# Kernel optimization log

Measured on AMD Instinct MI355X. Metric: run time of the kernel, lower is better.

## Reference

```python
import jax, jax.numpy as jnp
import numpy as np

HIDDEN = 1024
NUM_HEADS = 16
HEAD_SIZE = HIDDEN // NUM_HEADS
B, S = 2, 2048


def setup_inputs() -> dict:
    key = jax.random.key(0)
    k_x, k_wqkv, k_bqkv, k_wo, k_bo = jax.random.split(key, 5)
    x = jax.random.normal(k_x, (B, S, HIDDEN), dtype=jnp.float32)
    # Dense kernels, fan-in scaled like lecun_normal init
    Wqkv = jax.random.normal(k_wqkv, (HIDDEN, 3 * HIDDEN), dtype=jnp.float32) / np.sqrt(HIDDEN)
    bqkv = jnp.zeros((3 * HIDDEN,), dtype=jnp.float32)
    Wo = jax.random.normal(k_wo, (HIDDEN, HIDDEN), dtype=jnp.float32) / np.sqrt(HIDDEN)
    bo = jnp.zeros((HIDDEN,), dtype=jnp.float32)
    return {"x": x, "Wqkv": Wqkv, "bqkv": bqkv, "Wo": Wo, "bo": bo}


def reference(x, Wqkv, bqkv, Wo, bo):
    b, s, h = x.shape
    qkv = jnp.einsum('bsh,hf->bsf', x, Wqkv) + bqkv          # [b, s, 3*h]
    qkv = qkv.reshape(b, s, 3, NUM_HEADS, HEAD_SIZE)
    q, k, v = qkv[:, :, 0], qkv[:, :, 1], qkv[:, :, 2]        # [b, s, nh, hd]
    scale = 1.0 / np.sqrt(HEAD_SIZE)
    scores = jnp.einsum('bqhd,bkhd->bhqk', q, k) * scale      # [b, nh, s, s]
    weights = jax.nn.softmax(scores, axis=-1)
    attn = jnp.einsum('bhqk,bkhd->bqhd', weights, v)          # [b, s, nh, hd]
    attn = attn.reshape(b, s, h)
    return jnp.einsum('bsh,hf->bsf', attn, Wo) + bo
```

## Files before the change

### kernel.cpp

```cpp
#include <hip/hip_runtime.h>
#include <hip/hip_bf16.h>

#define HIDDEN 1024
#define NH 16
#define BATCH 2
#define SEQ 2048

typedef __attribute__((ext_vector_type(8))) short bf16x8;
typedef __attribute__((ext_vector_type(4))) float f32x4;

__device__ __forceinline__ ushort f2bf(float f) {
    __hip_bfloat16 h = __float2bfloat16(f);
    return *reinterpret_cast<ushort*>(&h);
}
__device__ __forceinline__ float bf2f(ushort u) {
    __hip_bfloat16 h;
    *reinterpret_cast<ushort*>(&h) = u;
    return __bfloat162float(h);
}

__device__ __forceinline__ void async_copy16(const ushort* g, ushort* l) {
    __builtin_amdgcn_global_load_lds((const __attribute__((address_space(1))) void*)g,
                                     (__attribute__((address_space(3))) void*)l,
                                     16, 0, 0);
}

__global__ void convert_f32_bf16_kernel(const float* __restrict__ in,
                                        ushort* __restrict__ out)
{
    int i = (blockIdx.x * 256 + threadIdx.x) * 4;
    float4 v = *(const float4*)(in + i);
    ushort4 w;
    w.x = f2bf(v.x); w.y = f2bf(v.y); w.z = f2bf(v.z); w.w = f2bf(v.w);
    *(ushort4*)(out + i) = w;
}

__global__ void transpose_f32_bf16_kernel(const float* __restrict__ W,
                                          ushort* __restrict__ Wt,
                                          int K, int N)
{
    __shared__ float t[32][33];
    int k0 = blockIdx.x * 32;
    int n0 = blockIdx.y * 32;
    int r = threadIdx.x >> 3;
    int c = (threadIdx.x & 7) * 4;
    float4 v = *(const float4*)(W + (size_t)(k0 + r) * N + n0 + c);
    t[r][c] = v.x; t[r][c + 1] = v.y; t[r][c + 2] = v.z; t[r][c + 3] = v.w;
    __syncthreads();
    ushort4 w;
    w.x = f2bf(t[c + 0][r]); w.y = f2bf(t[c + 1][r]);
    w.z = f2bf(t[c + 2][r]); w.w = f2bf(t[c + 3][r]);
    *(ushort4*)(Wt + (size_t)(n0 + r) * K + k0 + c) = w;
}

__global__ void transpose_split_bf16_kernel(const float* __restrict__ W,
                                            ushort* __restrict__ Wt_hi,
                                            ushort* __restrict__ Wt_lo,
                                            int K, int N)
{
    __shared__ float t[32][33];
    int k0 = blockIdx.x * 32;
    int n0 = blockIdx.y * 32;
    int r = threadIdx.x >> 3;
    int c = (threadIdx.x & 7) * 4;
    float4 v = *(const float4*)(W + (size_t)(k0 + r) * N + n0 + c);
    t[r][c] = v.x; t[r][c + 1] = v.y; t[r][c + 2] = v.z; t[r][c + 3] = v.w;
    __syncthreads();
    ushort4 whi, wlo;
    float vv;
    vv = t[c + 0][r]; whi.x = f2bf(vv); wlo.x = f2bf(vv - bf2f(whi.x));
    vv = t[c + 1][r]; whi.y = f2bf(vv); wlo.y = f2bf(vv - bf2f(whi.y));
    vv = t[c + 2][r]; whi.z = f2bf(vv); wlo.z = f2bf(vv - bf2f(whi.z));
    vv = t[c + 3][r]; whi.w = f2bf(vv); wlo.w = f2bf(vv - bf2f(whi.w));
    *(ushort4*)(Wt_hi + (size_t)(n0 + r) * K + k0 + c) = whi;
    *(ushort4*)(Wt_lo + (size_t)(n0 + r) * K + k0 + c) = wlo;
}

__global__ void transpose_v_kernel(const ushort* __restrict__ qkvb,
                                   ushort* __restrict__ vtg)
{
    __shared__ ushort T[64][72];
    int blk = blockIdx.x;
    int st = blk & 31;
    int h  = (blk >> 5) & 15;
    int b  = blk >> 9;
    int s0 = st * 64;

    int s  = threadIdx.x >> 2;
    int c0 = (threadIdx.x & 3) * 2;
    const ushort* src = qkvb + ((size_t)(b * SEQ + s0 + s)) * 3072 + 2048 + h * 64;
    *(uint4*)&T[s][c0 * 8]     = *(const uint4*)(src + c0 * 8);
    *(uint4*)&T[s][c0 * 8 + 8] = *(const uint4*)(src + c0 * 8 + 8);
    __syncthreads();

    int d = threadIdx.x >> 2;
    ushort* dst = vtg + ((size_t)((b * NH + h) * 64 + d)) * SEQ + s0;
    #pragma unroll
    for (int cc = 0; cc < 2; cc++) {
        int c2 = (threadIdx.x & 3) * 2 + cc;
        ushort tmp[8];
        #pragma unroll
        for (int j = 0; j < 8; j++) {
            int sp = c2 * 8 + j;
            int key = (sp & 3) * 16 + (sp >> 2);
            tmp[j] = T[key][d];
        }
        *(uint4*)(dst + c2 * 8) = *(const uint4*)tmp;
    }
}

__global__ __launch_bounds__(256, 3)
void gemm_mfma_bf16_kernel(const ushort* __restrict__ A,
                           const ushort* __restrict__ Bt,
                           const float* __restrict__ bias,
                           ushort* __restrict__ C, int N,
                           int qscale_cols)
{
    constexpr int K = 1024;
    __shared__ ushort As[128 * 64];
    __shared__ ushort Bs[128 * 64];

    const int tid  = threadIdx.x;
    const int wave = tid >> 6;
    const int lane = tid & 63;
    const int l16  = lane & 15;
    const int quad = lane >> 4;
    const int wm = wave & 1, wn = wave >> 1;

    const int bm = blockIdx.y * 128;
    const int bn = blockIdx.x * 128;

    const int srow = lane >> 3;
    const int lblk = (lane & 7) ^ srow;
    const ushort* Ag = A  + (size_t)(bm + wave * 32 + srow) * K + lblk * 8;
    const ushort* Bg = Bt + (size_t)(bn + wave * 32 + srow) * K + lblk * 8;
    ushort* Asl = As + wave * 32 * 64;
    ushort* Bsl = Bs + wave * 32 * 64;

    f32x4 acc[4][4];
    #pragma unroll
    for (int i = 0; i < 4; i++)
        #pragma unroll
        for (int j = 0; j < 4; j++) acc[i][j] = (f32x4){0.f, 0.f, 0.f, 0.f};

    for (int k0 = 0; k0 < K; k0 += 64) {
        __syncthreads();
        #pragma unroll
        for (int t = 0; t < 4; t++) {
            async_copy16(Ag + (size_t)t * 8 * K + k0, Asl + t * 8 * 64);
            async_copy16(Bg + (size_t)t * 8 * K + k0, Bsl + t * 8 * 64);
        }
        __syncthreads();

        #pragma unroll
        for (int s = 0; s < 2; s++) {
            bf16x8 af[4], bfr[4];
            #pragma unroll
            for (int i = 0; i < 4; i++) {
                int m = wm * 64 + i * 16 + l16;
                int n = wn * 64 + i * 16 + l16;
                af[i]  = *(const bf16x8*)&As[m * 64 + (((s * 4 + quad) ^ (m & 7)) << 3)];
                bfr[i] = *(const bf16x8*)&Bs[n * 64 + (((s * 4 + quad) ^ (n & 7)) << 3)];
            }
            #pragma unroll
            for (int i = 0; i < 4; i++)
                #pragma unroll
                for (int j = 0; j < 4; j++)
                    acc[i][j] = __builtin_amdgcn_mfma_f32_16x16x32_bf16(af[i], bfr[j], acc[i][j], 0, 0, 0);
        }
    }

    #pragma unroll
    for (int j = 0; j < 4; j++) {
        int col = bn + wn * 64 + j * 16 + l16;
        float bv = bias[col];
        float s = (col < qscale_cols) ? 0.125f : 1.0f;
        #pragma unroll
        for (int i = 0; i < 4; i++) {
            int row0 = bm + wm * 64 + i * 16 + quad * 4;
            #pragma unroll
            for (int r = 0; r < 4; r++)
                C[(size_t)(row0 + r) * N + col] = f2bf((acc[i][j][r] + bv) * s);
        }
    }
}

__global__ __launch_bounds__(256, 2)
void gemm3_split_kernel(const ushort* __restrict__ Ahi,
                        const ushort* __restrict__ Alo,
                        const ushort* __restrict__ Bthi,
                        const ushort* __restrict__ Btlo,
                        const float* __restrict__ bias,
                        float* __restrict__ C)
{
    constexpr int K = 1024, N = 1024;
    __shared__ ushort AsHi[128 * 64];
    __shared__ ushort AsLo[128 * 64];
    __shared__ ushort BsHi[64 * 64];
    __shared__ ushort BsLo[64 * 64];

    const int tid  = threadIdx.x;
    const int wave = tid >> 6;
    const int lane = tid & 63;
    const int l16  = lane & 15;
    const int quad = lane >> 4;
    const int wm = wave & 1, wn = wave >> 1;

    const int bm = blockIdx.y * 128;
    const int bn = blockIdx.x * 64;

    const int srow = lane >> 3;
    const int lblk = (lane & 7) ^ srow;
    const size_t aoff = (size_t)(bm + wave * 32 + srow) * K + lblk * 8;
    const size_t boff = (size_t)(bn + wave * 16 + srow) * K + lblk * 8;
    const ushort* AgHi = Ahi + aoff;
    const ushort* AgLo = Alo + aoff;
    const ushort* BgHi = Bthi + boff;
    const ushort* BgLo = Btlo + boff;
    ushort* AslHi = AsHi + wave * 32 * 64;
    ushort* AslLo = AsLo + wave * 32 * 64;
    ushort* BslHi = BsHi + wave * 16 * 64;
    ushort* BslLo = BsLo + wave * 16 * 64;

    f32x4 acc[4][2];
    #pragma unroll
    for (int i = 0; i < 4; i++)
        #pragma unroll
        for (int j = 0; j < 2; j++) acc[i][j] = (f32x4){0.f, 0.f, 0.f, 0.f};

    for (int k0 = 0; k0 < K; k0 += 64) {
        __syncthreads();
        #pragma unroll
        for (int t = 0; t < 4; t++) {
            async_copy16(AgHi + (size_t)t * 8 * K + k0, AslHi + t * 8 * 64);
            async_copy16(AgLo + (size_t)t * 8 * K + k0, AslLo + t * 8 * 64);
        }
        #pragma unroll
        for (int t = 0; t < 2; t++) {
            async_copy16(BgHi + (size_t)t * 8 * K + k0, BslHi + t * 8 * 64);
            async_copy16(BgLo + (size_t)t * 8 * K + k0, BslLo + t * 8 * 64);
        }
        __syncthreads();

        #pragma unroll
        for (int s = 0; s < 2; s++) {
            bf16x8 ah[4], al[4], bh[2], bl[2];
            #pragma unroll
            for (int i = 0; i < 4; i++) {
                int m = wm * 64 + i * 16 + l16;
                int idx = m * 64 + (((s * 4 + quad) ^ (m & 7)) << 3);
                ah[i] = *(const bf16x8*)&AsHi[idx];
                al[i] = *(const bf16x8*)&AsLo[idx];
            }
            #pragma unroll
            for (int j = 0; j < 2; j++) {
                int n = wn * 32 + j * 16 + l16;
                int idx = n * 64 + (((s * 4 + quad) ^ (n & 7)) << 3);
                bh[j] = *(const bf16x8*)&BsHi[idx];
                bl[j] = *(const bf16x8*)&BsLo[idx];
            }
            #pragma unroll
            for (int i = 0; i < 4; i++)
                #pragma unroll
                for (int j = 0; j < 2; j++) {
                    acc[i][j] = __builtin_amdgcn_mfma_f32_16x16x32_bf16(ah[i], bh[j], acc[i][j], 0, 0, 0);
                    acc[i][j] = __builtin_amdgcn_mfma_f32_16x16x32_bf16(ah[i], bl[j], acc[i][j], 0, 0, 0);
                    acc[i][j] = __builtin_amdgcn_mfma_f32_16x16x32_bf16(al[i], bh[j], acc[i][j], 0, 0, 0);
                }
        }
    }

    #pragma unroll
    for (int j = 0; j < 2; j++) {
        int col = bn + wn * 32 + j * 16 + l16;
        float bv = bias[col];
        #pragma unroll
        for (int i = 0; i < 4; i++) {
            int row0 = bm + wm * 64 + i * 16 + quad * 4;
            #pragma unroll
            for (int r = 0; r < 4; r++)
                C[(size_t)(row0 + r) * N + col] = acc[i][j][r] + bv;
        }
    }
}

__global__ __launch_bounds__(256, 2)
void attn_mfma_kernel(const ushort* __restrict__ qkvb,
                      const ushort* __restrict__ vtg,
                      int use_vtg,
                      ushort* __restrict__ attn_hi,
                      ushort* __restrict__ attn_lo)
{
    __shared__ ushort Ks[64 * 64];
    __shared__ ushort Vs[64 * 64];
    __shared__ ushort Ps[4][32 * 72];

    const int tid  = threadIdx.x;
    const int wave = tid >> 6;
    const int lane = tid & 63;
    const int l16  = lane & 15;
    const int quad = lane >> 4;

    const int qb = blockIdx.x & 15;
    const int bh = blockIdx.x >> 4;
    const int h  = bh & (NH - 1);
    const int b  = bh >> 4;

    const int qbase = qb * 128;
    const int hoff  = h * 64;

    bf16x8 a_q[2][2];
    #pragma unroll
    for (int mg = 0; mg < 2; mg++) {
        int qrow = b * SEQ + qbase + wave * 32 + mg * 16 + l16;
        const ushort* qp = qkvb + (size_t)qrow * 3072 + hoff + quad * 8;
        a_q[mg][0] = *(const bf16x8*)qp;
        a_q[mg][1] = *(const bf16x8*)(qp + 32);
    }

    f32x4 o[2][4];
    f32x4 lacc[2];
    #pragma unroll
    for (int mg = 0; mg < 2; mg++) {
        lacc[mg] = (f32x4){0.f, 0.f, 0.f, 0.f};
        #pragma unroll
        for (int nt = 0; nt < 4; nt++) o[mg][nt] = (f32x4){0.f, 0.f, 0.f, 0.f};
    }

    bf16x8 b_ones;
    #pragma unroll
    for (int j = 0; j < 8; j++) b_ones[j] = (short)0x3f80;

    const ushort* kvb    = qkvb + (size_t)b * SEQ * 3072;
    const ushort* vtg_bh = vtg + (size_t)((b * NH + h) * 64) * SEQ;

    for (int k0 = 0; k0 < SEQ; k0 += 64) {
        __syncthreads();
        if (use_vtg) {
            #pragma unroll
            for (int i = 0; i < 2; i++) {
                int row = (tid >> 3) + 32 * i;
                int blk = tid & 7;
                const ushort* ksrc = kvb + (size_t)(k0 + row) * 3072 + 1024 + hoff + blk * 8;
                uint4 kv = *(const uint4*)ksrc;
                *(uint4*)&Ks[row * 64 + ((blk ^ (row & 7)) << 3)] = kv;
                const ushort* vsrc = vtg_bh + (size_t)row * SEQ + k0 + blk * 8;
                uint4 vv = *(const uint4*)vsrc;
                *(uint4*)&Vs[row * 64 + ((blk ^ (row & 7)) << 3)] = vv;
            }
        } else {
            #pragma unroll
            for (int i = 0; i < 2; i++) {
                int key = (tid >> 3) + 32 * i;
                int blk = tid & 7;
                const ushort* ksrc = kvb + (size_t)(k0 + key) * 3072 + 1024 + hoff + blk * 8;
                uint4 kv = *(const uint4*)ksrc;
                *(uint4*)&Ks[key * 64 + ((blk ^ (key & 7)) << 3)] = kv;
                uint4 vv = *(const uint4*)(ksrc + 1024);
                const ushort* vp = (const ushort*)&vv;
                int pk_ = (key & 15) * 4 + (key >> 4);
                #pragma unroll
                for (int j = 0; j < 8; j++) {
                    int d = blk * 8 + j;
                    Vs[d * 64 + (((pk_ >> 3) ^ (d & 7)) << 3) + (pk_ & 7)] = vp[j];
                }
            }
        }
        __syncthreads();

        f32x4 sc[2][4];
        #pragma unroll
        for (int nt = 0; nt < 4; nt++) {
            int key = nt * 16 + l16;
            bf16x8 bk0 = *(const bf16x8*)&Ks[key * 64 + ((quad ^ (key & 7)) << 3)];
            bf16x8 bk1 = *(const bf16x8*)&Ks[key * 64 + (((4 + quad) ^ (key & 7)) << 3)];
            #pragma unroll
            for (int mg = 0; mg < 2; mg++) {
                f32x4 a = (f32x4){0.f, 0.f, 0.f, 0.f};
                a = __builtin_amdgcn_mfma_f32_16x16x32_bf16(a_q[mg][0], bk0, a, 0, 0, 0);
                a = __builtin_amdgcn_mfma_f32_16x16x32_bf16(a_q[mg][1], bk1, a, 0, 0, 0);
                sc[mg][nt] = a;
            }
        }

        #pragma unroll
        for (int mg = 0; mg < 2; mg++) {
            #pragma unroll
            for (int r = 0; r < 4; r++) {
                int q = mg * 16 + quad * 4 + r;
                uint2 pk2;
                pk2.x = (uint)f2bf(__expf(sc[mg][0][r])) |
                        ((uint)f2bf(__expf(sc[mg][1][r])) << 16);
                pk2.y = (uint)f2bf(__expf(sc[mg][2][r])) |
                        ((uint)f2bf(__expf(sc[mg][3][r])) << 16);
                *(uint2*)&Ps[wave][q * 72 + l16 * 4] = pk2;
            }
        }

        asm volatile("s_waitcnt lgkmcnt(0)" ::: "memory");
        bf16x8 a_p[2][2];
        #pragma unroll
        for (int mg = 0; mg < 2; mg++) {
            a_p[mg][0] = *(const bf16x8*)&Ps[wave][(mg * 16 + l16) * 72 + quad * 8];
            a_p[mg][1] = *(const bf16x8*)&Ps[wave][(mg * 16 + l16) * 72 + 32 + quad * 8];
        }

        #pragma unroll
        for (int nt = 0; nt < 4; nt++) {
            int d = nt * 16 + l16;
            bf16x8 bv0 = *(const bf16x8*)&Vs[d * 64 + ((quad ^ (d & 7)) << 3)];
            bf16x8 bv1 = *(const bf16x8*)&Vs[d * 64 + (((4 + quad) ^ (d & 7)) << 3)];
            #pragma unroll
            for (int mg = 0; mg < 2; mg++) {
                o[mg][nt] = __builtin_amdgcn_mfma_f32_16x16x32_bf16(a_p[mg][0], bv0, o[mg][nt], 0, 0, 0);
                o[mg][nt] = __builtin_amdgcn_mfma_f32_16x16x32_bf16(a_p[mg][1], bv1, o[mg][nt], 0, 0, 0);
            }
        }
        #pragma unroll
        for (int mg = 0; mg < 2; mg++) {
            lacc[mg] = __builtin_amdgcn_mfma_f32_16x16x32_bf16(a_p[mg][0], b_ones, lacc[mg], 0, 0, 0);
            lacc[mg] = __builtin_amdgcn_mfma_f32_16x16x32_bf16(a_p[mg][1], b_ones, lacc[mg], 0, 0, 0);
        }
    }

    #pragma unroll
    for (int mg = 0; mg < 2; mg++) {
        #pragma unroll
        for (int r = 0; r < 4; r++) {
            float inv = 1.f / lacc[mg][r];
            int row = b * SEQ + qbase + wave * 32 + mg * 16 + quad * 4 + r;
            size_t base = (size_t)row * HIDDEN + hoff + l16;
            #pragma unroll
            for (int nt = 0; nt < 4; nt++) {
                float val = o[mg][nt][r] * inv;
                ushort hi = f2bf(val);
                ushort lo = f2bf(val - bf2f(hi));
                attn_hi[base + nt * 16] = hi;
                attn_lo[base + nt * 16] = lo;
            }
        }
    }
}

extern "C" void kernel_launch(void* const* d_in, const int* in_sizes, int n_in,
                              void* d_out, int out_size, void* d_ws, size_t ws_size,
                              hipStream_t stream) {
    const float* x    = (const float*)d_in[0];
    const float* Wqkv = (const float*)d_in[1];
    const float* bqkv = (const float*)d_in[2];
    const float* Wo   = (const float*)d_in[3];
    const float* bo   = (const float*)d_in[4];
    float* out = (float*)d_out;

    const int M = BATCH * SEQ;
    const size_t MB = 1024 * 1024;

    char* ws = (char*)d_ws;
    ushort* qkvb    = (ushort*)ws;
    ushort* attn_hi = (ushort*)(ws + 24 * MB);
    ushort* attn_lo = (ushort*)(ws + 32 * MB);
    ushort* xb      = (ushort*)(ws + 24 * MB);
    ushort* Wt      = (ushort*)(ws + 32 * MB);
    ushort* WoT_hi  = (ushort*)(ws + 40 * MB);
    ushort* WoT_lo  = (ushort*)(ws + 42 * MB);
    ushort* vtg     = (ushort*)(ws + 44 * MB);
    const int use_vtg = (ws_size >= 52 * MB) ? 1 : 0;

    convert_f32_bf16_kernel<<<(M * HIDDEN) / 1024, 256, 0, stream>>>(x, xb);
    {
        dim3 grid(HIDDEN / 32, (3 * HIDDEN) / 32);
        transpose_f32_bf16_kernel<<<grid, 256, 0, stream>>>(Wqkv, Wt, HIDDEN, 3 * HIDDEN);
    }
    {
        dim3 grid(HIDDEN / 32, HIDDEN / 32);
        transpose_split_bf16_kernel<<<grid, 256, 0, stream>>>(Wo, WoT_hi, WoT_lo,
                                                              HIDDEN, HIDDEN);
    }

    {
        dim3 grid((3 * HIDDEN) / 128, M / 128);
        gemm_mfma_bf16_kernel<<<grid, 256, 0, stream>>>(xb, Wt, bqkv, qkvb,
                                                        3 * HIDDEN, HIDDEN);
    }

    if (use_vtg) {
        transpose_v_kernel<<<BATCH * NH * (SEQ / 64), 256, 0, stream>>>(qkvb, vtg);
    }

    attn_mfma_kernel<<<BATCH * NH * (SEQ / 128), 256, 0, stream>>>(qkvb, vtg, use_vtg,
                                                                   attn_hi, attn_lo);

    {
        dim3 grid(HIDDEN / 64, M / 128);
        gemm3_split_kernel<<<grid, 256, 0, stream>>>(attn_hi, attn_lo,
                                                     WoT_hi, WoT_lo, bo, out);
    }
}
```

Baseline: 203.8 us.

## Double-buffer attention K/V tiles with async LDS loads; merge prep kernels

```diff
diff --git a/kernel.cpp b/kernel.cpp
--- a/kernel.cpp
+++ b/kernel.cpp
@@ -25,55 +25,57 @@
                                      16, 0, 0);
 }
 
-__global__ void convert_f32_bf16_kernel(const float* __restrict__ in,
-                                        ushort* __restrict__ out)
-{
-    int i = (blockIdx.x * 256 + threadIdx.x) * 4;
-    float4 v = *(const float4*)(in + i);
-    ushort4 w;
-    w.x = f2bf(v.x); w.y = f2bf(v.y); w.z = f2bf(v.z); w.w = f2bf(v.w);
-    *(ushort4*)(out + i) = w;
-}
-
-__global__ void transpose_f32_bf16_kernel(const float* __restrict__ W,
-                                          ushort* __restrict__ Wt,
-                                          int K, int N)
+__global__ void prep_kernel(const float* __restrict__ x,
+                            const float* __restrict__ Wqkv,
+                            const float* __restrict__ Wo,
+                            ushort* __restrict__ xb,
+                            ushort* __restrict__ Wt,
+                            ushort* __restrict__ WoT_hi,
+                            ushort* __restrict__ WoT_lo)
 {
     __shared__ float t[32][33];
-    int k0 = blockIdx.x * 32;
-    int n0 = blockIdx.y * 32;
-    int r = threadIdx.x >> 3;
-    int c = (threadIdx.x & 7) * 4;
-    float4 v = *(const float4*)(W + (size_t)(k0 + r) * N + n0 + c);
-    t[r][c] = v.x; t[r][c + 1] = v.y; t[r][c + 2] = v.z; t[r][c + 3] = v.w;
-    __syncthreads();
-    ushort4 w;
-    w.x = f2bf(t[c + 0][r]); w.y = f2bf(t[c + 1][r]);
-    w.z = f2bf(t[c + 2][r]); w.w = f2bf(t[c + 3][r]);
-    *(ushort4*)(Wt + (size_t)(n0 + r) * K + k0 + c) = w;
-}
-
-__global__ void transpose_split_bf16_kernel(const float* __restrict__ W,
-                                            ushort* __restrict__ Wt_hi,
-                                            ushort* __restrict__ Wt_lo,
-                                            int K, int N)
-{
-    __shared__ float t[32][33];
-    int k0 = blockIdx.x * 32;
-    int n0 = blockIdx.y * 32;
-    int r = threadIdx.x >> 3;
-    int c = (threadIdx.x & 7) * 4;
-    float4 v = *(const float4*)(W + (size_t)(k0 + r) * N + n0 + c);
-    t[r][c] = v.x; t[r][c + 1] = v.y; t[r][c + 2] = v.z; t[r][c + 3] = v.w;
-    __syncthreads();
-    ushort4 whi, wlo;
-    float vv;
-    vv = t[c + 0][r]; whi.x = f2bf(vv); wlo.x = f2bf(vv - bf2f(whi.x));
-    vv = t[c + 1][r]; whi.y = f2bf(vv); wlo.y = f2bf(vv - bf2f(whi.y));
-    vv = t[c + 2][r]; whi.z = f2bf(vv); wlo.z = f2bf(vv - bf2f(whi.z));
-    vv = t[c + 3][r]; whi.w = f2bf(vv); wlo.w = f2bf(vv - bf2f(whi.w));
-    *(ushort4*)(Wt_hi + (size_t)(n0 + r) * K + k0 + c) = whi;
-    *(ushort4*)(Wt_lo + (size_t)(n0 + r) * K + k0 + c) = wlo;
+    const int bid = blockIdx.x;
+    const int tid = threadIdx.x;
+
+    if (bid < 4096) {
+        int i = (bid * 256 + tid) * 4;
+        float4 v = *(const float4*)(x + i);
+        ushort4 w;
+        w.x = f2bf(v.x); w.y = f2bf(v.y); w.z = f2bf(v.z); w.w = f2bf(v.w);
+        *(ushort4*)(xb + i) = w;
+        return;
+    }
+    const int r = tid >> 3;
+    const int c = (tid & 7) * 4;
+    if (bid < 7168) {
+        int tt = bid - 4096;
+        int k0 = (tt & 31) * 32;
+        int n0 = (tt >> 5) * 32;
+        const int N = 3 * HIDDEN, K = HIDDEN;
+        float4 v = *(const float4*)(Wqkv + (size_t)(k0 + r) * N + n0 + c);
+        t[r][c] = v.x; t[r][c + 1] = v.y; t[r][c + 2] = v.z; t[r][c + 3] = v.w;
+        __syncthreads();
+        ushort4 w;
+        w.x = f2bf(t[c + 0][r]); w.y = f2bf(t[c + 1][r]);
+        w.z = f2bf(t[c + 2][r]); w.w = f2bf(t[c + 3][r]);
+        *(ushort4*)(Wt + (size_t)(n0 + r) * K + k0 + c) = w;
+    } else {
+        int tt = bid - 7168;
+        int k0 = (tt & 31) * 32;
+        int n0 = (tt >> 5) * 32;
+        const int N = HIDDEN, K = HIDDEN;
+        float4 v = *(const float4*)(Wo + (size_t)(k0 + r) * N + n0 + c);
+        t[r][c] = v.x; t[r][c + 1] = v.y; t[r][c + 2] = v.z; t[r][c + 3] = v.w;
+        __syncthreads();
+        ushort4 whi, wlo;
+        float vv;
+        vv = t[c + 0][r]; whi.x = f2bf(vv); wlo.x = f2bf(vv - bf2f(whi.x));
+        vv = t[c + 1][r]; whi.y = f2bf(vv); wlo.y = f2bf(vv - bf2f(whi.y));
+        vv = t[c + 2][r]; whi.z = f2bf(vv); wlo.z = f2bf(vv - bf2f(whi.z));
+        vv = t[c + 3][r]; whi.w = f2bf(vv); wlo.w = f2bf(vv - bf2f(whi.w));
+        *(ushort4*)(WoT_hi + (size_t)(n0 + r) * K + k0 + c) = whi;
+        *(ushort4*)(WoT_lo + (size_t)(n0 + r) * K + k0 + c) = wlo;
+    }
 }
 
 __global__ void transpose_v_kernel(const ushort* __restrict__ qkvb,
@@ -291,8 +293,8 @@
                       ushort* __restrict__ attn_hi,
                       ushort* __restrict__ attn_lo)
 {
-    __shared__ ushort Ks[64 * 64];
-    __shared__ ushort Vs[64 * 64];
+    __shared__ ushort Ks[2][64 * 64];
+    __shared__ ushort Vs[2][64 * 64];
     __shared__ ushort Ps[4][32 * 72];
 
     const int tid  = threadIdx.x;
@@ -334,46 +336,64 @@
     const ushort* kvb    = qkvb + (size_t)b * SEQ * 3072;
     const ushort* vtg_bh = vtg + (size_t)((b * NH + h) * 64) * SEQ;
 
-    for (int k0 = 0; k0 < SEQ; k0 += 64) {
-        __syncthreads();
+    const int srow8 = lane >> 3;
+    const int sblk  = lane & 7;
+    const int gblk  = (sblk ^ srow8) << 3;
+    const ushort* kg = kvb + (size_t)(wave * 16 + srow8) * 3072 + 1024 + hoff + gblk;
+    const ushort* vg = vtg_bh + (size_t)(wave * 16 + srow8) * SEQ + gblk;
+
+    if (use_vtg) {
+        #pragma unroll
+        for (int c = 0; c < 2; c++) {
+            async_copy16(kg + (size_t)(c * 8) * 3072, &Ks[0][(wave * 16 + c * 8) * 64]);
+            async_copy16(vg + (size_t)(c * 8) * SEQ,  &Vs[0][(wave * 16 + c * 8) * 64]);
+        }
+    }
+
+    for (int t = 0; t < SEQ / 64; t++) {
+        const int k0 = t * 64;
+        const int cur = t & 1;
+
         if (use_vtg) {
-            #pragma unroll
-            for (int i = 0; i < 2; i++) {
-                int row = (tid >> 3) + 32 * i;
-                int blk = tid & 7;
-                const ushort* ksrc = kvb + (size_t)(k0 + row) * 3072 + 1024 + hoff + blk * 8;
-                uint4 kv = *(const uint4*)ksrc;
-                *(uint4*)&Ks[row * 64 + ((blk ^ (row & 7)) << 3)] = kv;
-                const ushort* vsrc = vtg_bh + (size_t)row * SEQ + k0 + blk * 8;
-                uint4 vv = *(const uint4*)vsrc;
-                *(uint4*)&Vs[row * 64 + ((blk ^ (row & 7)) << 3)] = vv;
+            asm volatile("s_waitcnt vmcnt(0)" ::: "memory");
+            asm volatile("s_barrier" ::: "memory");
+            if (t < SEQ / 64 - 1) {
+                const int nk0 = k0 + 64;
+                #pragma unroll
+                for (int c = 0; c < 2; c++) {
+                    async_copy16(kg + (size_t)(nk0 + c * 8) * 3072,
+                                 &Ks[cur ^ 1][(wave * 16 + c * 8) * 64]);
+                    async_copy16(vg + (size_t)(c * 8) * SEQ + nk0,
+                                 &Vs[cur ^ 1][(wave * 16 + c * 8) * 64]);
+                }
             }
         } else {
+            __syncthreads();
             #pragma unroll
             for (int i = 0; i < 2; i++) {
                 int key = (tid >> 3) + 32 * i;
                 int blk = tid & 7;
                 const ushort* ksrc = kvb + (size_t)(k0 + key) * 3072 + 1024 + hoff + blk * 8;
                 uint4 kv = *(const uint4*)ksrc;
-                *(uint4*)&Ks[key * 64 + ((blk ^ (key & 7)) << 3)] = kv;
+                *(uint4*)&Ks[cur][key * 64 + ((blk ^ (key & 7)) << 3)] = kv;
                 uint4 vv = *(const uint4*)(ksrc + 1024);
                 const ushort* vp = (const ushort*)&vv;
                 int pk_ = (key & 15) * 4 + (key >> 4);
                 #pragma unroll
                 for (int j = 0; j < 8; j++) {
                     int d = blk * 8 + j;
-                    Vs[d * 64 + (((pk_ >> 3) ^ (d & 7)) << 3) + (pk_ & 7)] = vp[j];
+                    Vs[cur][d * 64 + (((pk_ >> 3) ^ (d & 7)) << 3) + (pk_ & 7)] = vp[j];
                 }
             }
-        }
-        __syncthreads();
+            __syncthreads();
+        }
 
         f32x4 sc[2][4];
         #pragma unroll
         for (int nt = 0; nt < 4; nt++) {
             int key = nt * 16 + l16;
-            bf16x8 bk0 = *(const bf16x8*)&Ks[key * 64 + ((quad ^ (key & 7)) << 3)];
-            bf16x8 bk1 = *(const bf16x8*)&Ks[key * 64 + (((4 + quad) ^ (key & 7)) << 3)];
+            bf16x8 bk0 = *(const bf16x8*)&Ks[cur][key * 64 + ((quad ^ (key & 7)) << 3)];
+            bf16x8 bk1 = *(const bf16x8*)&Ks[cur][key * 64 + (((4 + quad) ^ (key & 7)) << 3)];
             #pragma unroll
             for (int mg = 0; mg < 2; mg++) {
                 f32x4 a = (f32x4){0.f, 0.f, 0.f, 0.f};
@@ -408,8 +428,8 @@
         #pragma unroll
         for (int nt = 0; nt < 4; nt++) {
             int d = nt * 16 + l16;
-            bf16x8 bv0 = *(const bf16x8*)&Vs[d * 64 + ((quad ^ (d & 7)) << 3)];
-            bf16x8 bv1 = *(const bf16x8*)&Vs[d * 64 + (((4 + quad) ^ (d & 7)) << 3)];
+            bf16x8 bv0 = *(const bf16x8*)&Vs[cur][d * 64 + ((quad ^ (d & 7)) << 3)];
+            bf16x8 bv1 = *(const bf16x8*)&Vs[cur][d * 64 + (((4 + quad) ^ (d & 7)) << 3)];
             #pragma unroll
             for (int mg = 0; mg < 2; mg++) {
                 o[mg][nt] = __builtin_amdgcn_mfma_f32_16x16x32_bf16(a_p[mg][0], bv0, o[mg][nt], 0, 0, 0);
@@ -466,16 +486,7 @@
     ushort* vtg     = (ushort*)(ws + 44 * MB);
     const int use_vtg = (ws_size >= 52 * MB) ? 1 : 0;
 
-    convert_f32_bf16_kernel<<<(M * HIDDEN) / 1024, 256, 0, stream>>>(x, xb);
-    {
-        dim3 grid(HIDDEN / 32, (3 * HIDDEN) / 32);
-        transpose_f32_bf16_kernel<<<grid, 256, 0, stream>>>(Wqkv, Wt, HIDDEN, 3 * HIDDEN);
-    }
-    {
-        dim3 grid(HIDDEN / 32, HIDDEN / 32);
-        transpose_split_bf16_kernel<<<grid, 256, 0, stream>>>(Wo, WoT_hi, WoT_lo,
-                                                              HIDDEN, HIDDEN);
-    }
+    prep_kernel<<<8192, 256, 0, stream>>>(x, Wqkv, Wo, xb, Wt, WoT_hi, WoT_lo);
 
     {
         dim3 grid((3 * HIDDEN) / 128, M / 128);
```

New measurement: 207.1 us. Within noise of the previous version (+1.6%).
